# Performance work log

Hardware: AMD Instinct MI355X
Metric: run time of the kernel (lower is better)

Reference implementation:

```python
import jax, jax.numpy as jnp
import numpy as np

EMBED_DIM = 1024
NUM_HEADS = 16
HEAD_DIM = EMBED_DIM // NUM_HEADS


def setup_inputs() -> dict:
    key = jax.random.key(0)
    ks = jax.random.split(key, 11)
    B, S, E = 4, 2048, EMBED_DIM
    s = 1.0 / np.sqrt(E)
    return {
        "query": jax.random.normal(ks[0], (B, S, E), jnp.float32),
        "key": jax.random.normal(ks[1], (B, S, E), jnp.float32),
        "value": jax.random.normal(ks[2], (B, S, E), jnp.float32),
        "Wq": jax.random.normal(ks[3], (E, E), jnp.float32) * s,
        "bq": jnp.zeros((E,), jnp.float32),
        "Wk": jax.random.normal(ks[4], (E, E), jnp.float32) * s,
        "bk": jnp.zeros((E,), jnp.float32),
        "Wv": jax.random.normal(ks[5], (E, E), jnp.float32) * s,
        "bv": jnp.zeros((E,), jnp.float32),
        "Wo": jax.random.normal(ks[6], (E, E), jnp.float32) * s,
        "bo": jnp.zeros((E,), jnp.float32),
    }


def reference(query, key, value, Wq, bq, Wk, bk, Wv, bv, Wo, bo):
    B, S, E = query.shape
    H, D = NUM_HEADS, HEAD_DIM
    scale = jnp.float32(np.sqrt(D))
    # linear projections (torch Linear: x @ W.T + b)
    Q = (query @ Wq.T + bq).reshape(B, S, H, D).transpose(0, 2, 1, 3)  # [B,H,S,D]
    K = (key @ Wk.T + bk).reshape(B, S, H, D).transpose(0, 2, 1, 3)
    V = (value @ Wv.T + bv).reshape(B, S, H, D).transpose(0, 2, 1, 3)
    # full O(S^2) score materialization, matching the eager torch code
    scores = jnp.einsum("bhqd,bhkd->bhqk", Q, K) / scale  # [B,H,S,S]
    attn = jax.nn.softmax(scores, axis=-1)
    out = jnp.einsum("bhqk,bhkd->bhqd", attn, V)  # [B,H,S,D]
    out = out.transpose(0, 2, 1, 3).reshape(B, S, E)
    out = out @ Wo.T + bo
    return out, attn.mean(axis=1)
```

## Files before the change

kernel.cpp:

```cpp
#include <hip/hip_runtime.h>
#include <hip/hip_bf16.h>

#define DEVI __device__ __forceinline__

typedef __bf16 bf16x8 __attribute__((ext_vector_type(8)));
typedef __bf16 bf16x4 __attribute__((ext_vector_type(4)));
typedef float f32x4 __attribute__((ext_vector_type(4)));

constexpr int B_ = 4, S_ = 2048, E_ = 1024, H_ = 16, D_ = 64;
constexpr int N_ = B_ * S_;
constexpr float SC2_ = 0.18033688011112042f;

constexpr size_t XB_OFF = 0;
constexpr size_t WB_OFF = 50331648;
constexpr size_t QB_OFF = 58720256;
constexpr size_t KB_OFF = 75497472;
constexpr size_t VT_OFF = 92274688;
constexpr size_t CTX_OFF = 109051904;
constexpr size_t LS_OFF = 125829120;
constexpr size_t WS_NEED = 126353408;

typedef const __attribute__((address_space(1))) void* gas_ptr;
typedef __attribute__((address_space(3))) void* las_ptr;

DEVI void load_lds16(const void* g, void* l) {
  __builtin_amdgcn_global_load_lds((gas_ptr)g, (las_ptr)l, 16, 0, 0);
}

DEVI f32x4 mfma16(bf16x8 a, bf16x8 b, f32x4 c) {
  return __builtin_amdgcn_mfma_f32_16x16x32_bf16(a, b, c, 0, 0, 0);
}

DEVI int swz(int row) { return ((row >> 1) ^ (row >> 3)) & 3; }

#if __has_builtin(__builtin_amdgcn_exp2f)
DEVI float ex2(float x) { return __builtin_amdgcn_exp2f(x); }
#else
DEVI float ex2(float x) { return exp2f(x); }
#endif

__global__ __launch_bounds__(256) void conv_all(const float* __restrict__ q,
                                                const float* __restrict__ k,
                                                const float* __restrict__ v,
                                                const float* __restrict__ wq,
                                                const float* __restrict__ wk,
                                                const float* __restrict__ wv,
                                                const float* __restrict__ wo,
                                                __bf16* __restrict__ dstx,
                                                __bf16* __restrict__ dstw) {
  const int bid = blockIdx.x;
  const float* src;
  __bf16* d;
  int sub;
  if (bid < 24576) {
    int part = bid >> 13;
    sub = bid & 8191;
    src = (part == 0) ? q : ((part == 1) ? k : v);
    d = dstx + (size_t)part * N_ * E_;
  } else {
    int wb = bid - 24576;
    int part = wb >> 10;
    sub = wb & 1023;
    src = (part == 0) ? wq : ((part == 1) ? wk : ((part == 2) ? wv : wo));
    d = dstw + (size_t)part * E_ * E_;
  }
  size_t i = ((size_t)sub * blockDim.x + threadIdx.x) * 4;
  float4 f = *(const float4*)(src + i);
  bf16x4 o;
  o[0] = (__bf16)f.x; o[1] = (__bf16)f.y; o[2] = (__bf16)f.z; o[3] = (__bf16)f.w;
  *(bf16x4*)(d + i) = o;
}

__global__ __launch_bounds__(256) void gemm_qkv(const __bf16* __restrict__ Xb,
                                                const __bf16* __restrict__ Wb,
                                                const float* __restrict__ bq,
                                                const float* __restrict__ bk,
                                                const float* __restrict__ bv,
                                                __bf16* __restrict__ Qb,
                                                __bf16* __restrict__ Kb,
                                                __bf16* __restrict__ Vt) {
  __shared__ __attribute__((aligned(16))) __bf16 As[128 * 32];
  __shared__ __attribute__((aligned(16))) __bf16 Bs[128 * 32];
  const int z = blockIdx.z;
  const __bf16* A = Xb + (size_t)z * N_ * E_;
  const __bf16* W = Wb + (size_t)z * E_ * E_;
  const float* bias = (z == 0) ? bq : ((z == 1) ? bk : bv);
  const int m0 = blockIdx.x * 128, n0 = blockIdx.y * 128;
  const int t = threadIdx.x, lane = t & 63, w = t >> 6;
  const int wm = w >> 1, wn = w & 1;
  const int l15 = lane & 15, g = lane >> 4;

  f32x4 acc[4][4] = {};

  for (int kk = 0; kk < E_; kk += 32) {
#pragma unroll
    for (int i = 0; i < 2; ++i) {
      int c = t + i * 256;
      int row = c >> 2, kc = c & 3;
      int sl = kc ^ swz(row);
      load_lds16(A + (size_t)(m0 + row) * E_ + kk + sl * 8, (void*)(As + c * 8));
      load_lds16(W + (size_t)(n0 + row) * E_ + kk + sl * 8, (void*)(Bs + c * 8));
    }
    __syncthreads();
    bf16x8 a[4], b[4];
#pragma unroll
    for (int i = 0; i < 4; ++i) {
      int row = wm * 64 + i * 16 + l15;
      a[i] = *(const bf16x8*)(As + row * 32 + (g ^ swz(row)) * 8);
    }
#pragma unroll
    for (int j = 0; j < 4; ++j) {
      int row = wn * 64 + j * 16 + l15;
      b[j] = *(const bf16x8*)(Bs + row * 32 + (g ^ swz(row)) * 8);
    }
#pragma unroll
    for (int i = 0; i < 4; ++i)
#pragma unroll
      for (int j = 0; j < 4; ++j)
        acc[i][j] = mfma16(a[i], b[j], acc[i][j]);
    __syncthreads();
  }

  const float oscale = (z == 0) ? SC2_ : 1.0f;
#pragma unroll
  for (int i = 0; i < 4; ++i) {
    int mloc = wm * 64 + i * 16 + (g << 2);
#pragma unroll
    for (int j = 0; j < 4; ++j) {
      int nloc = wn * 64 + j * 16 + l15;
      int n = n0 + nloc;
      int h = n >> 6, d = n & 63;
      float bs = bias[n];
      if (z == 2) {
        int m = m0 + mloc;
        int bb = m >> 11, s = m & 2047;
        bf16x4 pk;
#pragma unroll
        for (int r = 0; r < 4; ++r) pk[r] = (__bf16)(acc[i][j][r] + bs);
        *(bf16x4*)(Vt + ((size_t)(bb * H_ + h) * D_ + d) * S_ + s) = pk;
      } else {
        __bf16* dst = (z == 0) ? Qb : Kb;
#pragma unroll
        for (int r = 0; r < 4; ++r) {
          int m = m0 + mloc + r;
          int bb = m >> 11, s = m & 2047;
          dst[((size_t)(bb * H_ + h) * S_ + s) * D_ + d] = (__bf16)((acc[i][j][r] + bs) * oscale);
        }
      }
    }
  }
}

__global__ __launch_bounds__(256, 4) void attn_pv(const __bf16* __restrict__ Qb,
                                                  const __bf16* __restrict__ Kb,
                                                  const __bf16* __restrict__ Vt,
                                                  float* __restrict__ Lsum,
                                                  __bf16* __restrict__ Ctx) {
  __shared__ __attribute__((aligned(16))) __bf16 smem[2][8192];

  const int q0 = blockIdx.x * 128;
  const int bh = blockIdx.y;
  const __bf16* Qh = Qb + (size_t)bh * S_ * D_;
  const __bf16* Kh = Kb + (size_t)bh * S_ * D_;
  const __bf16* Vh = Vt + (size_t)bh * D_ * S_;
  const int t = threadIdx.x, lane = t & 63, w = t >> 6;
  const int l15 = lane & 15, g = lane >> 4;
  const int ksel = 8 * (l15 >> 2) + (l15 & 3);

  bf16x8 qf[2][2];
#pragma unroll
  for (int jb = 0; jb < 2; ++jb) {
    int row = w * 32 + jb * 16 + l15;
#pragma unroll
    for (int ks = 0; ks < 2; ++ks)
      qf[jb][ks] = *(const bf16x8*)(Qh + (size_t)(q0 + row) * D_ + ks * 32 + g * 8);
  }

  bf16x8 ones;
#pragma unroll
  for (int i = 0; i < 8; ++i) ones[i] = (__bf16)1.0f;

  f32x4 acc[4][2] = {};
  f32x4 lacc[2] = {};

  auto stage_kv = [&](int kk0, __bf16* buf) {
#pragma unroll
    for (int i = 0; i < 2; ++i) {
      int c = t + i * 256;
      int sub = c >> 8, rem = c & 255, row = rem >> 2, kc = rem & 3;
      int sl = kc ^ swz(row);
      load_lds16(Kh + (size_t)(kk0 + row) * D_ + sub * 32 + sl * 8, (void*)(buf + c * 8));
      load_lds16(Vh + (size_t)row * S_ + kk0 + sub * 32 + sl * 8, (void*)(buf + 4096 + c * 8));
    }
  };

  auto compute = [&](const __bf16* Ksb) {
    const __bf16* Vsb = Ksb + 4096;
#pragma unroll
    for (int chunk = 0; chunk < 2; ++chunk) {
      f32x4 sc[2][2];
#pragma unroll
      for (int blk = 0; blk < 2; ++blk) {
        int krow = chunk * 32 + 4 * blk + ksel;
        int so = (g ^ swz(krow)) * 8;
        bf16x8 kf0 = *(const bf16x8*)(Ksb + krow * 32 + so);
        bf16x8 kf1 = *(const bf16x8*)(Ksb + 2048 + krow * 32 + so);
#pragma unroll
        for (int jb = 0; jb < 2; ++jb) {
          f32x4 s = {};
          s = mfma16(kf0, qf[jb][0], s);
          s = mfma16(kf1, qf[jb][1], s);
          sc[blk][jb] = s;
        }
      }
      bf16x8 pf[2];
#pragma unroll
      for (int jb = 0; jb < 2; ++jb) {
#pragma unroll
        for (int r = 0; r < 4; ++r) {
          pf[jb][r]     = (__bf16)ex2(sc[0][jb][r]);
          pf[jb][4 + r] = (__bf16)ex2(sc[1][jb][r]);
        }
        lacc[jb] = mfma16(ones, pf[jb], lacc[jb]);
      }
      __builtin_amdgcn_s_setprio(1);
#pragma unroll
      for (int mb = 0; mb < 4; ++mb) {
        int row = mb * 16 + l15;
        bf16x8 vf = *(const bf16x8*)(Vsb + chunk * 2048 + row * 32 + (g ^ swz(row)) * 8);
#pragma unroll
        for (int jb = 0; jb < 2; ++jb)
          acc[mb][jb] = mfma16(vf, pf[jb], acc[mb][jb]);
      }
      __builtin_amdgcn_s_setprio(0);
    }
  };

  stage_kv(0, smem[0]);
  stage_kv(64, smem[1]);

  for (int tt = 0; tt < 30; ++tt) {
    asm volatile("s_waitcnt vmcnt(4)" ::: "memory");
    __builtin_amdgcn_s_barrier();
    compute(smem[tt & 1]);
    __builtin_amdgcn_s_barrier();
    stage_kv((tt + 2) * 64, smem[tt & 1]);
  }
  asm volatile("s_waitcnt vmcnt(4)" ::: "memory");
  __builtin_amdgcn_s_barrier();
  compute(smem[0]);
  asm volatile("s_waitcnt vmcnt(0)" ::: "memory");
  __builtin_amdgcn_s_barrier();
  compute(smem[1]);

  if (lane < 16) {
#pragma unroll
    for (int jb = 0; jb < 2; ++jb)
      Lsum[(size_t)bh * S_ + q0 + w * 32 + jb * 16 + lane] = lacc[jb][0];
  }

  const int bb = bh >> 4, h = bh & 15;
#pragma unroll
  for (int jb = 0; jb < 2; ++jb) {
    float invl = 1.0f / lacc[jb][0];
    int q = q0 + w * 32 + jb * 16 + l15;
#pragma unroll
    for (int mb = 0; mb < 4; ++mb) {
      int d = mb * 16 + (g << 2);
      bf16x4 pk;
#pragma unroll
      for (int r = 0; r < 4; ++r) pk[r] = (__bf16)(acc[mb][jb][r] * invl);
      *(bf16x4*)(Ctx + ((size_t)bb * S_ + q) * E_ + h * 64 + d) = pk;
    }
  }
}


DEVI void attn_mean_body(int id, __bf16* smem,
                         const __bf16* __restrict__ Qb,
                         const __bf16* __restrict__ Kb,
                         const float* __restrict__ Lsum,
                         float* __restrict__ meanout) {
  const int k0 = (id & 15) * 128;
  const int q0 = ((id >> 4) & 15) * 128;
  const int bI = id >> 8;
  const int t = threadIdx.x, lane = t & 63, w = t >> 6;
  const int l15 = lane & 15, g = lane >> 4;
  const int ksel = 8 * (l15 >> 2) + (l15 & 3);

  const __bf16* Qbase = Qb + (size_t)bI * H_ * S_ * D_;
  const __bf16* Kbase = Kb + (size_t)bI * H_ * S_ * D_;
  const float* Lbase = Lsum + (size_t)bI * H_ * S_;
  const int qrow0 = q0 + w * 32 + l15;

  f32x4 macc[4][2][2] = {};

  auto stage_k = [&](int h, __bf16* buf) {
    const __bf16* Kh = Kbase + (size_t)h * S_ * D_;
#pragma unroll
    for (int i = 0; i < 4; ++i) {
      int c = t + i * 256;
      int sub = c >> 9, rem = c & 511, row = rem >> 2, kc = rem & 3;
      int sl = kc ^ swz(row);
      load_lds16(Kh + (size_t)(k0 + row) * D_ + sub * 32 + sl * 8, (void*)(buf + c * 8));
    }
  };

  stage_k(0, smem);
  bf16x8 qf[2][2];
  float lraw[2];
#pragma unroll
  for (int jb = 0; jb < 2; ++jb) {
#pragma unroll
    for (int ks = 0; ks < 2; ++ks)
      qf[jb][ks] = *(const bf16x8*)(Qbase + (size_t)(qrow0 + jb * 16) * D_ + ks * 32 + g * 8);
    lraw[jb] = Lbase[qrow0 + jb * 16];
  }

  for (int h = 0; h < H_; ++h) {
    __bf16* cur = (h & 1) ? (smem + 8192) : smem;
    __bf16* nxt = (h & 1) ? smem : (smem + 8192);

    asm volatile("s_waitcnt vmcnt(0)" ::: "memory");
    __builtin_amdgcn_s_barrier();

    bf16x8 qfn[2][2];
    float lrawn[2];
    if (h + 1 < H_) {
      const __bf16* Qn = Qbase + (size_t)(h + 1) * S_ * D_;
#pragma unroll
      for (int jb = 0; jb < 2; ++jb) {
#pragma unroll
        for (int ks = 0; ks < 2; ++ks)
          qfn[jb][ks] = *(const bf16x8*)(Qn + (size_t)(qrow0 + jb * 16) * D_ + ks * 32 + g * 8);
        lrawn[jb] = Lbase[(size_t)(h + 1) * S_ + qrow0 + jb * 16];
      }
      stage_k(h + 1, nxt);
    }
    __builtin_amdgcn_sched_barrier(0);

    float invl[2];
#pragma unroll
    for (int jb = 0; jb < 2; ++jb) invl[jb] = 1.0f / lraw[jb];

#pragma unroll
    for (int chunk = 0; chunk < 4; ++chunk) {
#pragma unroll
      for (int blk = 0; blk < 2; ++blk) {
        int krow = chunk * 32 + 4 * blk + ksel;
        int so = (g ^ swz(krow)) * 8;
        bf16x8 kf0 = *(const bf16x8*)(cur + krow * 32 + so);
        bf16x8 kf1 = *(const bf16x8*)(cur + 4096 + krow * 32 + so);
#pragma unroll
        for (int jb = 0; jb < 2; ++jb) {
          f32x4 s = {};
          s = mfma16(kf0, qf[jb][0], s);
          s = mfma16(kf1, qf[jb][1], s);
#pragma unroll
          for (int r = 0; r < 4; ++r)
            macc[chunk][blk][jb][r] += ex2(s[r]) * invl[jb];
        }
      }
    }

    if (h + 1 < H_) {
#pragma unroll
      for (int jb = 0; jb < 2; ++jb) {
#pragma unroll
        for (int ks = 0; ks < 2; ++ks) qf[jb][ks] = qfn[jb][ks];
        lraw[jb] = lrawn[jb];
      }
    }
  }

#pragma unroll
  for (int chunk = 0; chunk < 4; ++chunk)
#pragma unroll
    for (int blk = 0; blk < 2; ++blk)
#pragma unroll
      for (int jb = 0; jb < 2; ++jb) {
        int q = q0 + w * 32 + jb * 16 + l15;
        int kb = k0 + chunk * 32 + 8 * g + 4 * blk;
        f32x4 o;
#pragma unroll
        for (int r = 0; r < 4; ++r) o[r] = macc[chunk][blk][jb][r] * 0.0625f;
        *(f32x4*)(meanout + ((size_t)bI * S_ + q) * S_ + kb) = o;
      }
}

DEVI void gemm_out_body(int id, __bf16* smem,
                        const __bf16* __restrict__ Ctx,
                        const __bf16* __restrict__ Wo,
                        const float* __restrict__ bo,
                        float* __restrict__ out) {
  __bf16* As = smem;
  __bf16* Bs = smem + 4096;
  const int m0 = (id & 63) * 128, n0 = (id >> 6) * 128;
  const int t = threadIdx.x, lane = t & 63, w = t >> 6;
  const int wm = w >> 1, wn = w & 1;
  const int l15 = lane & 15, g = lane >> 4;

  f32x4 acc[4][4] = {};

  for (int kk = 0; kk < E_; kk += 32) {
#pragma unroll
    for (int i = 0; i < 2; ++i) {
      int c = t + i * 256;
      int row = c >> 2, kc = c & 3;
      int sl = kc ^ swz(row);
      load_lds16(Ctx + (size_t)(m0 + row) * E_ + kk + sl * 8, (void*)(As + c * 8));
      load_lds16(Wo + (size_t)(n0 + row) * E_ + kk + sl * 8, (void*)(Bs + c * 8));
    }
    __syncthreads();
    bf16x8 a[4], b[4];
#pragma unroll
    for (int i = 0; i < 4; ++i) {
      int row = wm * 64 + i * 16 + l15;
      a[i] = *(const bf16x8*)(As + row * 32 + (g ^ swz(row)) * 8);
    }
#pragma unroll
    for (int j = 0; j < 4; ++j) {
      int row = wn * 64 + j * 16 + l15;
      b[j] = *(const bf16x8*)(Bs + row * 32 + (g ^ swz(row)) * 8);
    }
#pragma unroll
    for (int i = 0; i < 4; ++i)
#pragma unroll
      for (int j = 0; j < 4; ++j)
        acc[i][j] = mfma16(a[i], b[j], acc[i][j]);
    __syncthreads();
  }

#pragma unroll
  for (int i = 0; i < 4; ++i) {
    int mloc = wm * 64 + i * 16 + (g << 2);
#pragma unroll
    for (int j = 0; j < 4; ++j) {
      int n = n0 + wn * 64 + j * 16 + l15;
      float bs = bo[n];
#pragma unroll
      for (int r = 0; r < 4; ++r)
        out[(size_t)(m0 + mloc + r) * E_ + n] = acc[i][j][r] + bs;
    }
  }
}

__global__ __launch_bounds__(256, 3) void tail_fused(const __bf16* __restrict__ Qb,
                                                     const __bf16* __restrict__ Kb,
                                                     const float* __restrict__ Lsum,
                                                     float* __restrict__ meanout,
                                                     const __bf16* __restrict__ Ctx,
                                                     const __bf16* __restrict__ Wo,
                                                     const float* __restrict__ bo,
                                                     float* __restrict__ out) {
  __shared__ __attribute__((aligned(16))) __bf16 smem[16384];
  const int bid = blockIdx.x;
  const int g3 = bid / 3, r3 = bid - g3 * 3;
  if (r3 == 2)
    gemm_out_body(g3, smem, Ctx, Wo, bo, out);
  else
    attn_mean_body(2 * g3 + r3, smem, Qb, Kb, Lsum, meanout);
}

extern "C" void kernel_launch(void* const* d_in, const int* in_sizes, int n_in,
                              void* d_out, int out_size, void* d_ws, size_t ws_size,
                              hipStream_t stream) {
  if (ws_size < WS_NEED) {
    hipMemsetAsync(d_out, 0, (size_t)out_size * sizeof(float), stream);
    return;
  }

  const float* q  = (const float*)d_in[0];
  const float* k  = (const float*)d_in[1];
  const float* v  = (const float*)d_in[2];
  const float* Wq = (const float*)d_in[3];
  const float* bq = (const float*)d_in[4];
  const float* Wk = (const float*)d_in[5];
  const float* bk = (const float*)d_in[6];
  const float* Wv = (const float*)d_in[7];
  const float* bv = (const float*)d_in[8];
  const float* Wo = (const float*)d_in[9];
  const float* bo = (const float*)d_in[10];

  char* ws = (char*)d_ws;
  __bf16* Xb  = (__bf16*)(ws + XB_OFF);
  __bf16* Wb  = (__bf16*)(ws + WB_OFF);
  __bf16* Qb  = (__bf16*)(ws + QB_OFF);
  __bf16* Kb  = (__bf16*)(ws + KB_OFF);
  __bf16* Vt  = (__bf16*)(ws + VT_OFF);
  __bf16* Ctx = (__bf16*)(ws + CTX_OFF);
  float*  Ls  = (float*)(ws + LS_OFF);

  float* out0 = (float*)d_out;
  float* out1 = (float*)d_out + (size_t)N_ * E_;

  conv_all<<<dim3(28672), 256, 0, stream>>>(q, k, v, Wq, Wk, Wv, Wo, Xb, Wb);
  gemm_qkv<<<dim3(N_ / 128, E_ / 128, 3), 256, 0, stream>>>(Xb, Wb, bq, bk, bv, Qb, Kb, Vt);
  attn_pv<<<dim3(S_ / 128, B_ * H_), 256, 0, stream>>>(Qb, Kb, Vt, Ls, Ctx);
  tail_fused<<<dim3(1536), 256, 0, stream>>>(Qb, Kb, Ls, out1, Ctx,
                                             Wb + 3 * (size_t)E_ * E_, bo, out0);
}
```

Measured before the change: 411.1 us.

## Shrink attention-mean tiles to 32x128 and load K fragments directly into registers

```diff
diff --git a/kernel.cpp b/kernel.cpp
--- a/kernel.cpp
+++ b/kernel.cpp
@@ -276,38 +276,27 @@
 }
 
 
-DEVI void attn_mean_body(int id, __bf16* smem,
+DEVI void attn_mean_body(int id,
                          const __bf16* __restrict__ Qb,
                          const __bf16* __restrict__ Kb,
                          const float* __restrict__ Lsum,
                          float* __restrict__ meanout) {
   const int k0 = (id & 15) * 128;
-  const int q0 = ((id >> 4) & 15) * 128;
-  const int bI = id >> 8;
+  const int q0 = ((id >> 4) & 63) * 32;
+  const int bI = id >> 10;
   const int t = threadIdx.x, lane = t & 63, w = t >> 6;
   const int l15 = lane & 15, g = lane >> 4;
   const int ksel = 8 * (l15 >> 2) + (l15 & 3);
 
   const __bf16* Qbase = Qb + (size_t)bI * H_ * S_ * D_;
-  const __bf16* Kbase = Kb + (size_t)bI * H_ * S_ * D_;
+  const __bf16* Kbase = Kb + (size_t)bI * H_ * S_ * D_
+                        + (size_t)(k0 + w * 32 + ksel) * D_ + g * 8;
   const float* Lbase = Lsum + (size_t)bI * H_ * S_;
-  const int qrow0 = q0 + w * 32 + l15;
-
-  f32x4 macc[4][2][2] = {};
-
-  auto stage_k = [&](int h, __bf16* buf) {
-    const __bf16* Kh = Kbase + (size_t)h * S_ * D_;
-#pragma unroll
-    for (int i = 0; i < 4; ++i) {
-      int c = t + i * 256;
-      int sub = c >> 9, rem = c & 511, row = rem >> 2, kc = rem & 3;
-      int sl = kc ^ swz(row);
-      load_lds16(Kh + (size_t)(k0 + row) * D_ + sub * 32 + sl * 8, (void*)(buf + c * 8));
-    }
-  };
-
-  stage_k(0, smem);
-  bf16x8 qf[2][2];
+  const int qrow0 = q0 + l15;
+
+  f32x4 macc[2][2] = {};
+
+  bf16x8 qf[2][2], kf[2][2];
   float lraw[2];
 #pragma unroll
   for (int jb = 0; jb < 2; ++jb) {
@@ -316,18 +305,18 @@
       qf[jb][ks] = *(const bf16x8*)(Qbase + (size_t)(qrow0 + jb * 16) * D_ + ks * 32 + g * 8);
     lraw[jb] = Lbase[qrow0 + jb * 16];
   }
+#pragma unroll
+  for (int blk = 0; blk < 2; ++blk) {
+    kf[blk][0] = *(const bf16x8*)(Kbase + blk * 4 * D_);
+    kf[blk][1] = *(const bf16x8*)(Kbase + blk * 4 * D_ + 32);
+  }
 
   for (int h = 0; h < H_; ++h) {
-    __bf16* cur = (h & 1) ? (smem + 8192) : smem;
-    __bf16* nxt = (h & 1) ? smem : (smem + 8192);
-
-    asm volatile("s_waitcnt vmcnt(0)" ::: "memory");
-    __builtin_amdgcn_s_barrier();
-
-    bf16x8 qfn[2][2];
+    bf16x8 qfn[2][2], kfn[2][2];
     float lrawn[2];
     if (h + 1 < H_) {
       const __bf16* Qn = Qbase + (size_t)(h + 1) * S_ * D_;
+      const __bf16* Kn = Kbase + (size_t)(h + 1) * S_ * D_;
 #pragma unroll
       for (int jb = 0; jb < 2; ++jb) {
 #pragma unroll
@@ -335,7 +324,11 @@
           qfn[jb][ks] = *(const bf16x8*)(Qn + (size_t)(qrow0 + jb * 16) * D_ + ks * 32 + g * 8);
         lrawn[jb] = Lbase[(size_t)(h + 1) * S_ + qrow0 + jb * 16];
       }
-      stage_k(h + 1, nxt);
+#pragma unroll
+      for (int blk = 0; blk < 2; ++blk) {
+        kfn[blk][0] = *(const bf16x8*)(Kn + blk * 4 * D_);
+        kfn[blk][1] = *(const bf16x8*)(Kn + blk * 4 * D_ + 32);
+      }
     }
     __builtin_amdgcn_sched_barrier(0);
 
@@ -344,48 +337,41 @@
     for (int jb = 0; jb < 2; ++jb) invl[jb] = 1.0f / lraw[jb];
 
 #pragma unroll
-    for (int chunk = 0; chunk < 4; ++chunk) {
+    for (int blk = 0; blk < 2; ++blk)
+#pragma unroll
+      for (int jb = 0; jb < 2; ++jb) {
+        f32x4 s = {};
+        s = mfma16(kf[blk][0], qf[jb][0], s);
+        s = mfma16(kf[blk][1], qf[jb][1], s);
+#pragma unroll
+        for (int r = 0; r < 4; ++r)
+          macc[blk][jb][r] += ex2(s[r]) * invl[jb];
+      }
+
+    if (h + 1 < H_) {
+#pragma unroll
+      for (int jb = 0; jb < 2; ++jb) {
+        qf[jb][0] = qfn[jb][0]; qf[jb][1] = qfn[jb][1];
+        lraw[jb] = lrawn[jb];
+      }
 #pragma unroll
       for (int blk = 0; blk < 2; ++blk) {
-        int krow = chunk * 32 + 4 * blk + ksel;
-        int so = (g ^ swz(krow)) * 8;
-        bf16x8 kf0 = *(const bf16x8*)(cur + krow * 32 + so);
-        bf16x8 kf1 = *(const bf16x8*)(cur + 4096 + krow * 32 + so);
-#pragma unroll
-        for (int jb = 0; jb < 2; ++jb) {
-          f32x4 s = {};
-          s = mfma16(kf0, qf[jb][0], s);
-          s = mfma16(kf1, qf[jb][1], s);
-#pragma unroll
-          for (int r = 0; r < 4; ++r)
-            macc[chunk][blk][jb][r] += ex2(s[r]) * invl[jb];
-        }
-      }
-    }
-
-    if (h + 1 < H_) {
-#pragma unroll
-      for (int jb = 0; jb < 2; ++jb) {
-#pragma unroll
-        for (int ks = 0; ks < 2; ++ks) qf[jb][ks] = qfn[jb][ks];
-        lraw[jb] = lrawn[jb];
-      }
-    }
-  }
-
-#pragma unroll
-  for (int chunk = 0; chunk < 4; ++chunk)
-#pragma unroll
-    for (int blk = 0; blk < 2; ++blk)
-#pragma unroll
-      for (int jb = 0; jb < 2; ++jb) {
-        int q = q0 + w * 32 + jb * 16 + l15;
-        int kb = k0 + chunk * 32 + 8 * g + 4 * blk;
-        f32x4 o;
-#pragma unroll
-        for (int r = 0; r < 4; ++r) o[r] = macc[chunk][blk][jb][r] * 0.0625f;
-        *(f32x4*)(meanout + ((size_t)bI * S_ + q) * S_ + kb) = o;
-      }
+        kf[blk][0] = kfn[blk][0]; kf[blk][1] = kfn[blk][1];
+      }
+    }
+  }
+
+#pragma unroll
+  for (int blk = 0; blk < 2; ++blk)
+#pragma unroll
+    for (int jb = 0; jb < 2; ++jb) {
+      int q = q0 + jb * 16 + l15;
+      int kb = k0 + w * 32 + 8 * g + 4 * blk;
+      f32x4 o;
+#pragma unroll
+      for (int r = 0; r < 4; ++r) o[r] = macc[blk][jb][r] * 0.0625f;
+      *(f32x4*)(meanout + ((size_t)bI * S_ + q) * S_ + kb) = o;
+    }
 }
 
 DEVI void gemm_out_body(int id, __bf16* smem,
@@ -453,13 +439,13 @@
                                                      const __bf16* __restrict__ Wo,
                                                      const float* __restrict__ bo,
                                                      float* __restrict__ out) {
-  __shared__ __attribute__((aligned(16))) __bf16 smem[16384];
+  __shared__ __attribute__((aligned(16))) __bf16 smem[8192];
   const int bid = blockIdx.x;
-  const int g3 = bid / 3, r3 = bid - g3 * 3;
-  if (r3 == 2)
-    gemm_out_body(g3, smem, Ctx, Wo, bo, out);
+  const int g9 = bid / 9, r9 = bid - g9 * 9;
+  if (r9 == 8)
+    gemm_out_body(g9, smem, Ctx, Wo, bo, out);
   else
-    attn_mean_body(2 * g3 + r3, smem, Qb, Kb, Lsum, meanout);
+    attn_mean_body(g9 * 8 + r9, Qb, Kb, Lsum, meanout);
 }
 
 extern "C" void kernel_launch(void* const* d_in, const int* in_sizes, int n_in,
@@ -497,6 +483,6 @@
   conv_all<<<dim3(28672), 256, 0, stream>>>(q, k, v, Wq, Wk, Wv, Wo, Xb, Wb);
   gemm_qkv<<<dim3(N_ / 128, E_ / 128, 3), 256, 0, stream>>>(Xb, Wb, bq, bk, bv, Qb, Kb, Vt);
   attn_pv<<<dim3(S_ / 128, B_ * H_), 256, 0, stream>>>(Qb, Kb, Vt, Ls, Ctx);
-  tail_fused<<<dim3(1536), 256, 0, stream>>>(Qb, Kb, Ls, out1, Ctx,
+  tail_fused<<<dim3(4608), 256, 0, stream>>>(Qb, Kb, Ls, out1, Ctx,
                                              Wb + 3 * (size_t)E_ * E_, bo, out0);
 }
```

New measurement: 582.4 us. 1.42x slower.
